# Performance work log

Hardware: AMD Instinct MI355X
Metric: run time of the kernel (lower is better)

Reference implementation:

```python
import jax, jax.numpy as jnp
import numpy as np

EPS = 1e-6
RES_CONN = True


def _layernorm(x, g, b):
    mu = jnp.mean(x, axis=-1, keepdims=True)
    var = jnp.var(x, axis=-1, keepdims=True)
    return (x - mu) * jax.lax.rsqrt(var + EPS) * g + b


def setup_inputs() -> dict:
    key = jax.random.key(0)
    ks = jax.random.split(key, 8)
    L, H, V, B, T = 2, 1024, 32000, 4, 512
    s = 0.02
    return {
        "x": jax.random.randint(ks[0], (B, T), 0, V, dtype=jnp.int32),
        "emb": jax.random.normal(ks[1], (V, H), jnp.float32) * s,
        "ln_g": jnp.ones((L, H), jnp.float32),
        "ln_b": jnp.zeros((L, H), jnp.float32),
        "Wl": jax.random.normal(ks[2], (L, 2 * H, 4 * H), jnp.float32) * s,
        "bl": jnp.zeros((L, 4 * H), jnp.float32),
        "Wo": jax.random.normal(ks[3], (L, H, H), jnp.float32) * s,
        "bo": jnp.zeros((L, H), jnp.float32),
        "W1": jax.random.normal(ks[4], (L, H, 4 * H), jnp.float32) * s,
        "b1": jnp.zeros((L, 4 * H), jnp.float32),
        "W2": jax.random.normal(ks[5], (L, 4 * H, H), jnp.float32) * s,
        "b2": jnp.zeros((L, H), jnp.float32),
    }


def reference(x, emb, ln_g, ln_b, Wl, bl, Wo, bo, W1, b1, W2, b2):
    # x: [B, T] int token ids. Returns dec_logits [B, T, V].
    B, T = x.shape
    L, H = ln_g.shape
    x_emb = emb[x]                      # [B, T, H] (dropout inactive: eval mode)
    xs = jnp.swapaxes(x_emb, 0, 1)      # [T, B, H]

    def step(carry, xt):
        c_prev, h_prev = carry          # each [L, B, H]
        cs, hs = [], []
        prev_input = jnp.zeros_like(xt)
        inp = xt                        # [B, H]
        for m in range(L):
            xn = _layernorm(inp, ln_g[m], ln_b[m])
            z = jnp.concatenate([xn, h_prev[m]], axis=-1) @ Wl[m] + bl[m]
            z = z.reshape(B, 4, H)
            i_g = jax.nn.sigmoid(z[:, 0])
            f_g = jax.nn.sigmoid(z[:, 1])
            o_g = jax.nn.sigmoid(z[:, 2])
            c = f_g * c_prev[m] + i_g * jnp.tanh(z[:, 3])
            h = o_g * jnp.tanh(c)
            ff = jax.nn.relu(xn @ W1[m] + b1[m]) @ W2[m] + b2[m]
            y = inp + ff + h @ Wo[m] + bo[m]
            if RES_CONN:
                y = y + prev_input
            prev_input = inp
            inp = y
            cs.append(c)
            hs.append(h)
        logits = inp @ emb.T            # tied embedding: [B, V]
        return (jnp.stack(cs), jnp.stack(hs)), logits

    carry0 = (jnp.zeros((L, B, H), x_emb.dtype), jnp.zeros((L, B, H), x_emb.dtype))
    _, logits = jax.lax.scan(step, carry0, xs)   # logits [T, B, V]
    return jnp.swapaxes(logits, 0, 1)            # [B, T, V]
```

## Files before the change

### kernel.cpp

```cpp
#include <hip/hip_runtime.h>

typedef unsigned short u16;
typedef short bf16x8 __attribute__((ext_vector_type(8)));
typedef unsigned short ushort8 __attribute__((ext_vector_type(8)));
typedef unsigned short us4 __attribute__((ext_vector_type(4)));
typedef unsigned u32x4 __attribute__((ext_vector_type(4)));
typedef float fx4 __attribute__((ext_vector_type(4)));

#define DEVI __device__ __forceinline__

enum { BB = 4, TT = 512, HH = 1024, VV = 32000, H4 = 4096 };
enum { WSTR = 1032 };

DEVI u16 f2bf(float f) {
    union { float f; unsigned u; } x; x.f = f;
    unsigned r = x.u + 0x7fff + ((x.u >> 16) & 1);
    return (u16)(r >> 16);
}
DEVI float bf2f(u16 u) {
    union { unsigned u; float f; } x; x.u = ((unsigned)u) << 16;
    return x.f;
}
DEVI float sigm(float x) { return 1.f / (1.f + __expf(-x)); }
DEVI float tanh_f(float x) {
    float a = fabsf(x);
    float t = 1.f - 2.f / (__expf(2.f * a) + 1.f);
    return x < 0.f ? -t : t;
}

DEVI unsigned ald_u32(const unsigned* p) { return __hip_atomic_load(p, __ATOMIC_RELAXED, __HIP_MEMORY_SCOPE_AGENT); }
DEVI void ast_u32(unsigned* p, unsigned v) { __hip_atomic_store(p, v, __ATOMIC_RELAXED, __HIP_MEMORY_SCOPE_AGENT); }

DEVI void ld4cc(const unsigned* p, u32x4* out) {
    asm volatile("global_load_dwordx4 %0, %1, off sc0 sc1" : "=v"(*out) : "v"(p));
}

template <int SLP>
DEVI void sent_poll(const unsigned* sbase, unsigned want, int lane) {
    const unsigned* p = sbase + lane;
    unsigned v = ald_u32(p);
    while (v != want) { __builtin_amdgcn_s_sleep(SLP); v = ald_u32(p); }
}
DEVI void data_fetch(const unsigned* dbase, u16* st, int tid) {
    u32x4 d;
    ld4cc(dbase + tid * 4, &d);
    asm volatile("s_waitcnt vmcnt(0)" ::: "memory");
    __builtin_amdgcn_sched_barrier(0);
    int wi = tid * 8;
    u16* dst = st + (wi >> 10) * WSTR + (wi & 1023);
    *(us4*)dst       = (us4){(u16)d[0], (u16)(d[0] >> 16), (u16)d[1], (u16)(d[1] >> 16)};
    *(us4*)(dst + 4) = (us4){(u16)d[2], (u16)(d[2] >> 16), (u16)d[3], (u16)(d[3] >> 16)};
}

template <int SLP>
DEVI void poll4096(const unsigned* base, unsigned want, u16* st, int tid) {
    const unsigned* p0 = base + tid * 8;
    const unsigned* p1 = p0 + 4;
    u32x4 v0, v1;
    ld4cc(p0, &v0); ld4cc(p1, &v1);
    asm volatile("s_waitcnt vmcnt(0)" ::: "memory");
    __builtin_amdgcn_sched_barrier(0);
    for (;;) {
        bool o0 = ((v0[0]>>16)==want)&((v0[1]>>16)==want)&((v0[2]>>16)==want)&((v0[3]>>16)==want);
        bool o1 = ((v1[0]>>16)==want)&((v1[1]>>16)==want)&((v1[2]>>16)==want)&((v1[3]>>16)==want);
        if (o0 & o1) break;
        __builtin_amdgcn_s_sleep(SLP);
        if (!o0) ld4cc(p0, &v0);
        if (!o1) ld4cc(p1, &v1);
        asm volatile("s_waitcnt vmcnt(0)" ::: "memory");
        __builtin_amdgcn_sched_barrier(0);
    }
    int wi = tid * 8;
    u16* d = st + (wi >> 10) * WSTR + (wi & 1023);
    *(us4*)d       = (us4){(u16)v0[0], (u16)v0[1], (u16)v0[2], (u16)v0[3]};
    *(us4*)(d + 4) = (us4){(u16)v1[0], (u16)v1[1], (u16)v1[2], (u16)v1[3]};
}

DEVI unsigned poll_word(const unsigned* p, unsigned want) {
    unsigned v = ald_u32(p);
    while ((v >> 16) != want) { __builtin_amdgcn_s_sleep(2); v = ald_u32(p); }
    return v & 0xFFFFu;
}

DEVI void gates64(const u16* wl, const u16* st, float* fb, int tid) {
    int lane = tid & 63, wv = tid >> 6;
    int rt = wv & 3, kh = wv >> 2;
    fx4 acc = {0.f, 0.f, 0.f, 0.f};
    int aoff = (rt * 16 + (lane & 15)) * WSTR + (lane >> 4) * 8;
    int boff = (lane & 3) * WSTR + (lane >> 4) * 8;
#pragma unroll
    for (int kt = 0; kt < 16; kt++) {
        int k0 = (kh * 16 + kt) * 32;
        bf16x8 a = *(const bf16x8*)(wl + aoff + k0);
        bf16x8 b = *(const bf16x8*)(st + boff + k0);
        acc = __builtin_amdgcn_mfma_f32_16x16x32_bf16(a, b, acc, 0, 0, 0);
    }
    int col = lane & 15;
    if (col < 4) {
        int r0 = rt * 16 + (lane >> 4) * 4;
#pragma unroll
        for (int ri = 0; ri < 4; ri++) fb[kh * 256 + (r0 + ri) * 4 + col] = acc[ri];
    }
}

__global__ void transpose_cast(const float* __restrict__ src, u16* __restrict__ dst, int R, int C) {
    __shared__ float tile[32][33];
    int c0 = blockIdx.x * 32, r0 = blockIdx.y * 32;
    int x = threadIdx.x, y = threadIdx.y;
#pragma unroll
    for (int i = 0; i < 32; i += 8) tile[y + i][x] = src[(size_t)(r0 + y + i) * C + c0 + x];
    __syncthreads();
#pragma unroll
    for (int i = 0; i < 32; i += 8) dst[(size_t)(c0 + y + i) * R + r0 + x] = f2bf(tile[x][y + i]);
}

__global__ void cast_bf16(const float* __restrict__ src, u16* __restrict__ dst, int n) {
    int i = blockIdx.x * 256 + threadIdx.x;
    if (i < n) dst[i] = f2bf(src[i]);
}

__global__ void zero_buf(float* p, int n) {
    int i = blockIdx.x * 256 + threadIdx.x;
    if (i < n) p[i] = 0.f;
}

__global__ __launch_bounds__(256) void gather_ln(const int* __restrict__ x, const float* __restrict__ emb,
                                                 const float* __restrict__ g, const float* __restrict__ b,
                                                 float* __restrict__ xe, u16* __restrict__ xn0) {
    int t = blockIdx.x, bb = blockIdx.y;
    int row = x[bb * TT + t];
    const float* e = emb + (size_t)row * HH;
    float v[4]; float s = 0.f, s2 = 0.f;
#pragma unroll
    for (int p = 0; p < 4; p++) { v[p] = e[p * 256 + threadIdx.x]; s += v[p]; s2 += v[p] * v[p]; }
    __shared__ float ls[4], ls2[4];
    for (int off = 32; off; off >>= 1) { s += __shfl_xor(s, off); s2 += __shfl_xor(s2, off); }
    int w = threadIdx.x >> 6, lane = threadIdx.x & 63;
    if (lane == 0) { ls[w] = s; ls2[w] = s2; }
    __syncthreads();
    s = ls[0] + ls[1] + ls[2] + ls[3];
    s2 = ls2[0] + ls2[1] + ls2[2] + ls2[3];
    float mu = s * (1.f / HH);
    float var = s2 * (1.f / HH) - mu * mu;
    float rs = rsqrtf(var + 1e-6f);
    size_t base = ((size_t)t * BB + bb) * HH;
#pragma unroll
    for (int p = 0; p < 4; p++) {
        int j = p * 256 + threadIdx.x;
        xe[base + j] = v[p];
        xn0[base + j] = f2bf((v[p] - mu) * rs * g[j] + b[j]);
    }
}

template <int MODE>
__global__ __launch_bounds__(256) void gemm_bt(const u16* __restrict__ A, const u16* __restrict__ Bt,
                                               float* __restrict__ Cf, u16* __restrict__ Cb,
                                               const float* __restrict__ bias, int M, int N, int K) {
    __shared__ u16 ldsA[128 * 40];
    __shared__ u16 ldsB[128 * 40];
    const int tid = threadIdx.x;
    const int m0 = blockIdx.y * 128, n0 = blockIdx.x * 128;
    const int lane = tid & 63, wid = tid >> 6;
    const int wr = wid >> 1, wc = wid & 1;
    const int l15 = lane & 15, lk = (lane >> 4) * 8;
    fx4 acc[4][4];
#pragma unroll
    for (int a = 0; a < 4; a++)
#pragma unroll
        for (int b = 0; b < 4; b++) { fx4 z = {0.f, 0.f, 0.f, 0.f}; acc[a][b] = z; }

    const int arow = tid >> 2, acol = (tid & 3) * 8;
    for (int k0 = 0; k0 < K; k0 += 32) {
#pragma unroll
        for (int p = 0; p < 2; p++) {
            int r = arow + p * 64;
            ushort8 va = *(const ushort8*)(A + (size_t)(m0 + r) * K + k0 + acol);
            *(ushort8*)&ldsA[r * 40 + acol] = va;
            ushort8 vb = *(const ushort8*)(Bt + (size_t)(n0 + r) * K + k0 + acol);
            *(ushort8*)&ldsB[r * 40 + acol] = vb;
        }
        __syncthreads();
        bf16x8 af[4], bfr[4];
#pragma unroll
        for (int mi = 0; mi < 4; mi++) af[mi] = *(const bf16x8*)&ldsA[(wr * 64 + mi * 16 + l15) * 40 + lk];
#pragma unroll
        for (int ni = 0; ni < 4; ni++) bfr[ni] = *(const bf16x8*)&ldsB[(wc * 64 + ni * 16 + l15) * 40 + lk];
#pragma unroll
        for (int mi = 0; mi < 4; mi++)
#pragma unroll
            for (int ni = 0; ni < 4; ni++)
                acc[mi][ni] = __builtin_amdgcn_mfma_f32_16x16x32_bf16(af[mi], bfr[ni], acc[mi][ni], 0, 0, 0);
        __syncthreads();
    }
#pragma unroll
    for (int mi = 0; mi < 4; mi++) {
#pragma unroll
        for (int ni = 0; ni < 4; ni++) {
#pragma unroll
            for (int r = 0; r < 4; r++) {
                int gr = m0 + wr * 64 + mi * 16 + (lane >> 4) * 4 + r;
                int gc = n0 + wc * 64 + ni * 16 + l15;
                float v = acc[mi][ni][r];
                if (MODE == 0) {
                    Cf[(size_t)gr * N + gc] = v + bias[gc];
                } else if (MODE == 1) {
                    float u = v + bias[gc];
                    Cb[(size_t)gr * N + gc] = f2bf(u > 0.f ? u : 0.f);
                } else if (MODE == 2) {
                    Cf[(size_t)gr * N + gc] += v;
                } else {
                    int b = gr & 3, t = gr >> 2;
                    Cf[((size_t)b * TT + t) * VV + gc] = v;
                }
            }
        }
    }
}

__global__ __launch_bounds__(512, 1) void lstm_pipe(
    const u16* __restrict__ Wh0T, const u16* __restrict__ Wo0T,
    const u16* __restrict__ Wx1T, const u16* __restrict__ Wh1T,
    const float* __restrict__ pz_all, const float* __restrict__ xe, const float* __restrict__ ff0,
    const float* __restrict__ lng, const float* __restrict__ lnb,
    const float* __restrict__ bl, const float* __restrict__ bo,
    float* __restrict__ y0_all, u16* __restrict__ xn1, u16* __restrict__ H1bf,
    unsigned* __restrict__ R) {
    __shared__ u16 wlds[64 * WSTR];
    __shared__ u16 stg[4 * WSTR];
    __shared__ float fb[1664];

    const int bid = blockIdx.x;
    const int tid = threadIdx.x;
    const int lane = tid & 63, wv = tid >> 6;

    unsigned* RD0 = R;
    unsigned* RS0 = R + 32768;
    unsigned* RD1 = R + 33792;
    unsigned* RS1 = R + 41984;
    unsigned* RPART = R + 42240;
    unsigned* RXN = R + 46336;
    unsigned* RZX = R + 111872;
    unsigned* PROGY = R + 374016;
    unsigned* PROGZX = R + 376064;
    unsigned* PROGL1 = R + 378112;

    if (bid < 64) {
        const int w = bid;
        {
            int row = tid >> 3, kc = tid & 7;
            int gr = (row >> 4) * 1024 + w * 16 + (row & 15);
            const uint4* s = (const uint4*)(Wh0T + (size_t)gr * 1024 + kc * 128);
            uint4* d = (uint4*)(wlds + row * WSTR + kc * 128);
#pragma unroll
            for (int i = 0; i < 16; i++) d[i] = s[i];
        }
        if (tid < 64) fb[1024 + tid] = 0.f;
        __syncthreads();

        for (int s = 0; s < TT; s++) {
            if ((s & 7) == 0 && tid < 64) {
                for (;;) {
                    unsigned p = ald_u32(PROGY + tid * 32);
#pragma unroll
                    for (int off = 1; off < 64; off <<= 1) {
                        unsigned o = (unsigned)__shfl_xor((int)p, off);
                        p = p < o ? p : o;
                    }
                    if ((int)p >= s - 8) break;
                    __builtin_amdgcn_s_sleep(8);
                }
            }
            float pzv[4] = {0.f, 0.f, 0.f, 0.f};
            if (tid < 64) {
                int x = tid >> 2, b = tid & 3;
#pragma unroll
                for (int g = 0; g < 4; g++)
                    pzv[g] = pz_all[((size_t)s * 4 + b) * 4096 + g * 1024 + w * 16 + x];
            }
            if (wv == 0) sent_poll<1>(RS0 + ((s + 15) & 15) * 64, (unsigned)s, lane);
            __syncthreads();
            data_fetch(RD0 + ((s + 15) & 15) * 2048, stg, tid);
            __syncthreads();
            float* gbuf = fb + (s & 1) * 512;
            gates64(wlds, stg, gbuf, tid);
            __syncthreads();
            if (tid < 64) {
                int x = tid >> 2, b = tid & 3;
                float z0 = gbuf[(0*16+x)*4+b] + gbuf[256+(0*16+x)*4+b] + pzv[0];
                float z1 = gbuf[(1*16+x)*4+b] + gbuf[256+(1*16+x)*4+b] + pzv[1];
                float z2 = gbuf[(2*16+x)*4+b] + gbuf[256+(2*16+x)*4+b] + pzv[2];
                float z3 = gbuf[(3*16+x)*4+b] + gbuf[256+(3*16+x)*4+b] + pzv[3];
                float ig = sigm(z0), fg = sigm(z1), og = sigm(z2), gg = tanh_f(z3);
                float c = fg * fb[1024 + tid] + ig * gg;
                fb[1024 + tid] = c;
                float h = og * tanh_f(c);
                float hn = __shfl(h, (tid + 4) & 63);
                if (((tid >> 2) & 1) == 0) {
                    int x = tid >> 2, b = tid & 3;
                    unsigned word = (unsigned)f2bf(h) | ((unsigned)f2bf(hn) << 16);
                    ast_u32(&RD0[(s & 15) * 2048 + b * 512 + w * 8 + (x >> 1)], word);
                }
                asm volatile("s_waitcnt vmcnt(0)" ::: "memory");
                if (tid == 0) ast_u32(&RS0[(s & 15) * 64 + w], (unsigned)(s + 1));
            }
        }
    } else if (bid < 128) {
        const int wy = bid - 64;
        {
            int row = tid >> 5, kc = tid & 31;
            const uint4* s = (const uint4*)(Wo0T + (size_t)(wy * 16 + row) * 1024 + kc * 32);
            uint4* d = (uint4*)(wlds + row * WSTR + kc * 32);
            d[0] = s[0]; d[1] = s[1]; d[2] = s[2]; d[3] = s[3];
        }
        float lgR = 0.f, lbR = 0.f, boR = 0.f;
        if (tid < 64) {
            int x = tid >> 2;
            lgR = lng[1024 + wy * 16 + x];
            lbR = lnb[1024 + wy * 16 + x];
            boR = bo[wy * 16 + x];
        }
        __syncthreads();

        for (int t = 0; t <= TT; t++) {
            const bool doDot = (t < TT);
            const bool doLN = (t >= 1);
            if ((t & 7) == 0 && tid < 64) {
                for (;;) {
                    unsigned p = ald_u32(PROGZX + tid * 32);
#pragma unroll
                    for (int off = 1; off < 64; off <<= 1) {
                        unsigned o = (unsigned)__shfl_xor((int)p, off);
                        p = p < o ? p : o;
                    }
                    if ((int)p >= t - 8) break;
                    __builtin_amdgcn_s_sleep(8);
                }
            }
            float xev = 0.f, ffv = 0.f;
            if (doDot && tid < 64) {
                int x = tid >> 2, b = tid & 3;
                size_t base = ((size_t)t * 4 + b) * 1024 + wy * 16 + x;
                xev = xe[base]; ffv = ff0[base];
            }
            if (doDot && wv == 0) sent_poll<4>(RS0 + (t & 15) * 64, (unsigned)(t + 1), lane);
            __syncthreads();
            if (doDot) data_fetch(RD0 + (t & 15) * 2048, stg, tid);
            if (doLN) {
                const unsigned* p = RPART + ((t - 1) & 3) * 1024 + tid * 2;
                unsigned hi = poll_word(p, (unsigned)t);
                unsigned lo = poll_word(p + 1, (unsigned)t);
                union { unsigned u; float f; } cv; cv.u = (hi << 16) | lo;
                fb[tid] = cv.f;
            }
            __syncthreads();
            if (doDot && tid == 0) ast_u32(PROGY + wy * 32, (unsigned)(t + 1));
            if (doLN && tid < 8) {
                int b = tid & 3, kind = tid >> 2;
                float S = 0.f;
                for (int i = 0; i < 64; i++) S += fb[i * 8 + b * 2 + kind];
                fb[704 + kind * 4 + b] = S;
            }
            if (doDot) {
                int out = tid >> 3, c = tid & 7;
                const u16* wrow = wlds + (out >> 2) * WSTR + c * 128;
                const u16* hrow = stg + (out & 3) * WSTR + c * 128;
                float acc = 0.f;
#pragma unroll
                for (int m = 0; m < 16; m++) {
                    ushort8 w8 = *(const ushort8*)(wrow + m * 8);
                    ushort8 h8 = *(const ushort8*)(hrow + m * 8);
#pragma unroll
                    for (int q = 0; q < 8; q++) acc += bf2f(w8[q]) * bf2f(h8[q]);
                }
                acc += __shfl_xor(acc, 1); acc += __shfl_xor(acc, 2); acc += __shfl_xor(acc, 4);
                if (c == 0) fb[512 + out] = acc;
            }
            __syncthreads();
            if (doDot && tid < 64) {
                int x = tid >> 2, b = tid & 3;
                float y = fb[512 + tid] + xev + ffv + boR;
                y0_all[((size_t)t * 4 + b) * 1024 + wy * 16 + x] = y;
                fb[576 + (t & 1) * 64 + tid] = y;
                float sv = y, sq = y * y;
#pragma unroll
                for (int off = 4; off < 64; off <<= 1) { sv += __shfl_xor(sv, off); sq += __shfl_xor(sq, off); }
                if (tid < 4) {
                    unsigned tg = (unsigned)(t + 1) << 16;
                    unsigned* pb = RPART + (t & 3) * 1024 + wy * 16 + tid * 4;
                    union { float f; unsigned u; } c1, c2; c1.f = sv; c2.f = sq;
                    ast_u32(pb + 0, tg | (c1.u >> 16));
                    ast_u32(pb + 1, tg | (c1.u & 0xFFFFu));
                    ast_u32(pb + 2, tg | (c2.u >> 16));
                    ast_u32(pb + 3, tg | (c2.u & 0xFFFFu));
                }
            }
            __syncthreads();
            if (doLN && tid < 64) {
                int x = tid >> 2, b = tid & 3;
                int u = t - 1;
                float mu = fb[704 + b] * (1.f / 1024.f);
                float rs = rsqrtf(fb[708 + b] * (1.f / 1024.f) - mu * mu + 1e-6f);
                float yv = fb[576 + (u & 1) * 64 + tid];
                float xnv = (yv - mu) * rs * lgR + lbR;
                u16 xb = f2bf(xnv);
                xn1[(size_t)u * 4096 + b * 1024 + wy * 16 + x] = xb;
                ast_u32(&RXN[(u & 15) * 4096 + b * 1024 + wy * 16 + x],
                        ((unsigned)(u + 1) << 16) | xb);
            }
        }
    } else if (bid < 192) {
        const int wz = bid - 128;
        {
            int row = tid >> 3, kc = tid & 7;
            int gr = (row >> 4) * 1024 + wz * 16 + (row & 15);
            const uint4* s = (const uint4*)(Wx1T + (size_t)gr * 1024 + kc * 128);
            uint4* d = (uint4*)(wlds + row * WSTR + kc * 128);
#pragma unroll
            for (int i = 0; i < 16; i++) d[i] = s[i];
        }
        if (tid < 64) fb[1536 + tid] = bl[4096 + (tid >> 4) * 1024 + wz * 16 + (tid & 15)];
        __syncthreads();

        for (int t = 0; t < TT; t++) {
            if ((t & 7) == 0 && tid == 0) {
                while ((int)ald_u32(PROGL1) < t - 6) __builtin_amdgcn_s_sleep(8);
            }
            poll4096<8>(RXN + (t & 15) * 4096, (unsigned)(t + 1), stg, tid);
            __syncthreads();
            gates64(wlds, stg, fb, tid);
            __syncthreads();
            if (tid == 0) ast_u32(PROGZX + wz * 32, (unsigned)(t + 1));
            if (tid < 256) {
                int lr = tid >> 2, b = tid & 3;
                float v = fb[lr * 4 + b] + fb[256 + lr * 4 + b] + fb[1536 + lr];
                ast_u32(&RZX[(t & 15) * 16384 + wz * 256 + tid],
                        ((unsigned)(t + 1) << 16) | f2bf(v));
            }
            __syncthreads();
        }
    } else {
        const int w1 = bid - 192;
        {
            int row = tid >> 3, kc = tid & 7;
            int gr = (row >> 4) * 1024 + w1 * 16 + (row & 15);
            const uint4* s = (const uint4*)(Wh1T + (size_t)gr * 1024 + kc * 128);
            uint4* d = (uint4*)(wlds + row * WSTR + kc * 128);
#pragma unroll
            for (int i = 0; i < 16; i++) d[i] = s[i];
        }
        if (tid < 64) fb[1600 + tid] = 0.f;
        __syncthreads();

        for (int v = 0; v < TT; v++) {
            if (tid < 256) {
                const unsigned* p = RZX + (v & 15) * 16384 + w1 * 256 + tid;
                fb[1024 + (v & 1) * 256 + tid] = bf2f((u16)poll_word(p, (unsigned)(v + 1)));
            }
            if (wv == 0) sent_poll<1>(RS1 + ((v + 3) & 3) * 64, (unsigned)v, lane);
            __syncthreads();
            data_fetch(RD1 + ((v + 3) & 3) * 2048, stg, tid);
            __syncthreads();
            if (bid == 192 && tid == 0) ast_u32(PROGL1, (unsigned)(v + 1));
            float* gbuf = fb + (v & 1) * 512;
            gates64(wlds, stg, gbuf, tid);
            __syncthreads();
            if (tid < 64) {
                int x = tid >> 2, b = tid & 3;
                const float* zb = fb + 1024 + (v & 1) * 256;
                float z0 = gbuf[(0*16+x)*4+b] + gbuf[256+(0*16+x)*4+b] + zb[(0*16+x)*4+b];
                float z1 = gbuf[(1*16+x)*4+b] + gbuf[256+(1*16+x)*4+b] + zb[(1*16+x)*4+b];
                float z2 = gbuf[(2*16+x)*4+b] + gbuf[256+(2*16+x)*4+b] + zb[(2*16+x)*4+b];
                float z3 = gbuf[(3*16+x)*4+b] + gbuf[256+(3*16+x)*4+b] + zb[(3*16+x)*4+b];
                float ig = sigm(z0), fg = sigm(z1), og = sigm(z2), gg = tanh_f(z3);
                float c = fg * fb[1600 + tid] + ig * gg;
                fb[1600 + tid] = c;
                float h = og * tanh_f(c);
                u16 hb = f2bf(h);
                H1bf[(size_t)v * 4096 + b * 1024 + w1 * 16 + x] = hb;
                float hn = __shfl(h, (tid + 4) & 63);
                if (((tid >> 2) & 1) == 0) {
                    unsigned word = (unsigned)hb | ((unsigned)f2bf(hn) << 16);
                    ast_u32(&RD1[(v & 3) * 2048 + b * 512 + w1 * 8 + ((tid >> 2) >> 1)], word);
                }
                asm volatile("s_waitcnt vmcnt(0)" ::: "memory");
                if (tid == 0) ast_u32(&RS1[(v & 3) * 64 + w1], (unsigned)(v + 1));
            }
        }
    }
}

__global__ void p1_add(float* __restrict__ y, const float* __restrict__ xe,
                       const float* __restrict__ b2_1, const float* __restrict__ bo_1) {
    int idx = blockIdx.x * 256 + threadIdx.x;
    int j = idx & (HH - 1);
    y[idx] += xe[idx] + b2_1[j] + bo_1[j];
}

__global__ void p2_cast(const float* __restrict__ y, u16* __restrict__ o) {
    int idx = blockIdx.x * 256 + threadIdx.x;
    o[idx] = f2bf(y[idx]);
}

extern "C" void kernel_launch(void* const* d_in, const int* in_sizes, int n_in,
                              void* d_out, int out_size, void* d_ws, size_t ws_size,
                              hipStream_t stream) {
    const int* x = (const int*)d_in[0];
    const float* emb = (const float*)d_in[1];
    const float* ln_g = (const float*)d_in[2];
    const float* ln_b = (const float*)d_in[3];
    const float* Wl = (const float*)d_in[4];
    const float* bl = (const float*)d_in[5];
    const float* Wo = (const float*)d_in[6];
    const float* bo = (const float*)d_in[7];
    const float* W1 = (const float*)d_in[8];
    const float* b1 = (const float*)d_in[9];
    const float* W2 = (const float*)d_in[10];
    const float* b2 = (const float*)d_in[11];
    float* out = (float*)d_out;

    char* wp = (char*)d_ws;
    auto alloc = [&](size_t bytes) { void* p = wp; wp += (bytes + 255) & ~(size_t)255; return p; };
    const size_t MBT = (size_t)TT * BB;
    float* xe     = (float*)alloc(MBT * HH * 4);
    float* pre_z0 = (float*)alloc(MBT * H4 * 4);
    float* ff0    = (float*)alloc(MBT * HH * 4);
    float* y0_all = (float*)alloc(MBT * HH * 4);
    u16* xn0      = (u16*)alloc(MBT * HH * 2);
    u16* xn1      = (u16*)alloc(MBT * HH * 2);
    u16* U0       = (u16*)alloc(MBT * H4 * 2);
    u16* U1       = (u16*)alloc(MBT * H4 * 2);
    u16* H1bf     = (u16*)alloc(MBT * HH * 2);
    u16* Y1bf     = (u16*)alloc(MBT * HH * 2);
    unsigned* R   = (unsigned*)alloc(378144 * 4);
    u16* WlxT0 = (u16*)alloc((size_t)H4 * HH * 2);
    u16* WlhT0 = (u16*)alloc((size_t)H4 * HH * 2);
    u16* WlxT1 = (u16*)alloc((size_t)H4 * HH * 2);
    u16* WlhT1 = (u16*)alloc((size_t)H4 * HH * 2);
    u16* Wo0T  = (u16*)alloc((size_t)HH * HH * 2);
    u16* Wo1T  = (u16*)alloc((size_t)HH * HH * 2);
    u16* W10T  = (u16*)alloc((size_t)H4 * HH * 2);
    u16* W11T  = (u16*)alloc((size_t)H4 * HH * 2);
    u16* W20T  = (u16*)alloc((size_t)HH * H4 * 2);
    u16* W21T  = (u16*)alloc((size_t)HH * H4 * 2);
    u16* embB  = (u16*)alloc((size_t)VV * HH * 2);

    dim3 tb(32, 8);
    transpose_cast<<<dim3(128, 32), tb, 0, stream>>>(Wl, WlxT0, HH, H4);
    transpose_cast<<<dim3(128, 32), tb, 0, stream>>>(Wl + 1024 * 4096, WlhT0, HH, H4);
    transpose_cast<<<dim3(128, 32), tb, 0, stream>>>(Wl + 2048 * 4096, WlxT1, HH, H4);
    transpose_cast<<<dim3(128, 32), tb, 0, stream>>>(Wl + 3072 * 4096, WlhT1, HH, H4);
    transpose_cast<<<dim3(32, 32), tb, 0, stream>>>(Wo, Wo0T, HH, HH);
    transpose_cast<<<dim3(32, 32), tb, 0, stream>>>(Wo + 1024 * 1024, Wo1T, HH, HH);
    transpose_cast<<<dim3(128, 32), tb, 0, stream>>>(W1, W10T, HH, H4);
    transpose_cast<<<dim3(128, 32), tb, 0, stream>>>(W1 + 1024 * 4096, W11T, HH, H4);
    transpose_cast<<<dim3(32, 128), tb, 0, stream>>>(W2, W20T, H4, HH);
    transpose_cast<<<dim3(32, 128), tb, 0, stream>>>(W2 + 4096 * 1024, W21T, H4, HH);
    cast_bf16<<<(VV * HH + 255) / 256, 256, 0, stream>>>(emb, embB, VV * HH);
    gather_ln<<<dim3(TT, BB), 256, 0, stream>>>(x, emb, ln_g, ln_b, xe, xn0);

    gemm_bt<0><<<dim3(32, 16), 256, 0, stream>>>(xn0, WlxT0, pre_z0, nullptr, bl, 2048, 4096, 1024);
    gemm_bt<1><<<dim3(32, 16), 256, 0, stream>>>(xn0, W10T, nullptr, U0, b1, 2048, 4096, 1024);
    gemm_bt<0><<<dim3(8, 16), 256, 0, stream>>>(U0, W20T, ff0, nullptr, b2, 2048, 1024, 4096);

    zero_buf<<<1478, 256, 0, stream>>>((float*)R, 378144);

    lstm_pipe<<<256, 512, 0, stream>>>(WlhT0, Wo0T, WlxT1, WlhT1, pre_z0, xe, ff0,
                                       ln_g, ln_b, bl, bo, y0_all, xn1, H1bf, R);

    gemm_bt<1><<<dim3(32, 16), 256, 0, stream>>>(xn1, W11T, nullptr, U1, b1 + 4096, 2048, 4096, 1024);
    p1_add<<<8192, 256, 0, stream>>>(y0_all, xe, b2 + 1024, bo + 1024);
    gemm_bt<2><<<dim3(8, 16), 256, 0, stream>>>(U1, W21T, y0_all, nullptr, nullptr, 2048, 1024, 4096);
    gemm_bt<2><<<dim3(8, 16), 256, 0, stream>>>(H1bf, Wo1T, y0_all, nullptr, nullptr, 2048, 1024, 1024);
    p2_cast<<<8192, 256, 0, stream>>>(y0_all, Y1bf);
    gemm_bt<3><<<dim3(250, 16), 256, 0, stream>>>(Y1bf, embB, out, nullptr, nullptr, 2048, 32000, 1024);
}
```

Measured before the change: 3.641 ms.

## Use direct global-to-LDS loads in GEMM and fuse epilogue add/cast kernels

The GEMM tile loads now go straight from global memory into LDS via global_load_lds, dropping the register round-trip, and the padded LDS stride is removed. Two elementwise kernels are removed: the residual/bias add moves into the W2 GEMM epilogue, and the bf16 cast of y moves into the Wo GEMM epilogue. The LSTM progress polling now uses wave 1 instead of wave 0, presumably so it overlaps with the wave 0 sentinel poll. Without the LDS padding, the MFMA fragment reads may hit more bank conflicts.

```diff
diff --git a/kernel.cpp b/kernel.cpp
--- a/kernel.cpp
+++ b/kernel.cpp
@@ -33,6 +33,11 @@
 
 DEVI void ld4cc(const unsigned* p, u32x4* out) {
     asm volatile("global_load_dwordx4 %0, %1, off sc0 sc1" : "=v"(*out) : "v"(p));
+}
+
+DEVI void gl_lds16(const u16* g, u16* l) {
+    __builtin_amdgcn_global_load_lds((const __attribute__((address_space(1))) unsigned*)g,
+                                     (__attribute__((address_space(3))) unsigned*)l, 16, 0, 0);
 }
 
 template <int SLP>
@@ -155,9 +160,10 @@
 template <int MODE>
 __global__ __launch_bounds__(256) void gemm_bt(const u16* __restrict__ A, const u16* __restrict__ Bt,
                                                float* __restrict__ Cf, u16* __restrict__ Cb,
-                                               const float* __restrict__ bias, int M, int N, int K) {
-    __shared__ u16 ldsA[128 * 40];
-    __shared__ u16 ldsB[128 * 40];
+                                               const float* __restrict__ bias, const float* __restrict__ bias2,
+                                               const float* __restrict__ addf, int M, int N, int K) {
+    __shared__ u16 ldsA[128 * 32];
+    __shared__ u16 ldsB[128 * 32];
     const int tid = threadIdx.x;
     const int m0 = blockIdx.y * 128, n0 = blockIdx.x * 128;
     const int lane = tid & 63, wid = tid >> 6;
@@ -169,22 +175,19 @@
 #pragma unroll
         for (int b = 0; b < 4; b++) { fx4 z = {0.f, 0.f, 0.f, 0.f}; acc[a][b] = z; }
 
-    const int arow = tid >> 2, acol = (tid & 3) * 8;
+    const int srow = lane >> 2, scol = (lane & 3) * 8;
+    const int i0 = wid * 32;
     for (int k0 = 0; k0 < K; k0 += 32) {
-#pragma unroll
-        for (int p = 0; p < 2; p++) {
-            int r = arow + p * 64;
-            ushort8 va = *(const ushort8*)(A + (size_t)(m0 + r) * K + k0 + acol);
-            *(ushort8*)&ldsA[r * 40 + acol] = va;
-            ushort8 vb = *(const ushort8*)(Bt + (size_t)(n0 + r) * K + k0 + acol);
-            *(ushort8*)&ldsB[r * 40 + acol] = vb;
-        }
+        gl_lds16(A + (size_t)(m0 + i0 + srow) * K + k0 + scol,       &ldsA[i0 * 32]);
+        gl_lds16(A + (size_t)(m0 + i0 + 16 + srow) * K + k0 + scol,  &ldsA[(i0 + 16) * 32]);
+        gl_lds16(Bt + (size_t)(n0 + i0 + srow) * K + k0 + scol,      &ldsB[i0 * 32]);
+        gl_lds16(Bt + (size_t)(n0 + i0 + 16 + srow) * K + k0 + scol, &ldsB[(i0 + 16) * 32]);
         __syncthreads();
         bf16x8 af[4], bfr[4];
 #pragma unroll
-        for (int mi = 0; mi < 4; mi++) af[mi] = *(const bf16x8*)&ldsA[(wr * 64 + mi * 16 + l15) * 40 + lk];
-#pragma unroll
-        for (int ni = 0; ni < 4; ni++) bfr[ni] = *(const bf16x8*)&ldsB[(wc * 64 + ni * 16 + l15) * 40 + lk];
+        for (int mi = 0; mi < 4; mi++) af[mi] = *(const bf16x8*)&ldsA[(wr * 64 + mi * 16 + l15) * 32 + lk];
+#pragma unroll
+        for (int ni = 0; ni < 4; ni++) bfr[ni] = *(const bf16x8*)&ldsB[(wc * 64 + ni * 16 + l15) * 32 + lk];
 #pragma unroll
         for (int mi = 0; mi < 4; mi++)
 #pragma unroll
@@ -201,16 +204,19 @@
                 int gr = m0 + wr * 64 + mi * 16 + (lane >> 4) * 4 + r;
                 int gc = n0 + wc * 64 + ni * 16 + l15;
                 float v = acc[mi][ni][r];
+                size_t idx = (size_t)gr * N + gc;
                 if (MODE == 0) {
-                    Cf[(size_t)gr * N + gc] = v + bias[gc];
+                    Cf[idx] = v + bias[gc];
                 } else if (MODE == 1) {
                     float u = v + bias[gc];
-                    Cb[(size_t)gr * N + gc] = f2bf(u > 0.f ? u : 0.f);
-                } else if (MODE == 2) {
-                    Cf[(size_t)gr * N + gc] += v;
-                } else {
+                    Cb[idx] = f2bf(u > 0.f ? u : 0.f);
+                } else if (MODE == 3) {
                     int b = gr & 3, t = gr >> 2;
                     Cf[((size_t)b * TT + t) * VV + gc] = v;
+                } else if (MODE == 4) {
+                    Cf[idx] += v + addf[idx] + bias[gc] + bias2[gc];
+                } else {
+                    Cb[idx] = f2bf(Cf[idx] + v);
                 }
             }
         }
@@ -258,9 +264,9 @@
         __syncthreads();
 
         for (int s = 0; s < TT; s++) {
-            if ((s & 7) == 0 && tid < 64) {
+            if ((s & 7) == 0 && wv == 1) {
                 for (;;) {
-                    unsigned p = ald_u32(PROGY + tid * 32);
+                    unsigned p = ald_u32(PROGY + lane * 32);
 #pragma unroll
                     for (int off = 1; off < 64; off <<= 1) {
                         unsigned o = (unsigned)__shfl_xor((int)p, off);
@@ -296,7 +302,6 @@
                 float h = og * tanh_f(c);
                 float hn = __shfl(h, (tid + 4) & 63);
                 if (((tid >> 2) & 1) == 0) {
-                    int x = tid >> 2, b = tid & 3;
                     unsigned word = (unsigned)f2bf(h) | ((unsigned)f2bf(hn) << 16);
                     ast_u32(&RD0[(s & 15) * 2048 + b * 512 + w * 8 + (x >> 1)], word);
                 }
@@ -324,9 +329,9 @@
         for (int t = 0; t <= TT; t++) {
             const bool doDot = (t < TT);
             const bool doLN = (t >= 1);
-            if ((t & 7) == 0 && tid < 64) {
+            if ((t & 7) == 0 && wv == 1) {
                 for (;;) {
-                    unsigned p = ald_u32(PROGZX + tid * 32);
+                    unsigned p = ald_u32(PROGZX + lane * 32);
 #pragma unroll
                     for (int off = 1; off < 64; off <<= 1) {
                         unsigned o = (unsigned)__shfl_xor((int)p, off);
@@ -487,18 +492,6 @@
             }
         }
     }
-}
-
-__global__ void p1_add(float* __restrict__ y, const float* __restrict__ xe,
-                       const float* __restrict__ b2_1, const float* __restrict__ bo_1) {
-    int idx = blockIdx.x * 256 + threadIdx.x;
-    int j = idx & (HH - 1);
-    y[idx] += xe[idx] + b2_1[j] + bo_1[j];
-}
-
-__global__ void p2_cast(const float* __restrict__ y, u16* __restrict__ o) {
-    int idx = blockIdx.x * 256 + threadIdx.x;
-    o[idx] = f2bf(y[idx]);
 }
 
 extern "C" void kernel_launch(void* const* d_in, const int* in_sizes, int n_in,
@@ -558,19 +551,17 @@
     cast_bf16<<<(VV * HH + 255) / 256, 256, 0, stream>>>(emb, embB, VV * HH);
     gather_ln<<<dim3(TT, BB), 256, 0, stream>>>(x, emb, ln_g, ln_b, xe, xn0);
 
-    gemm_bt<0><<<dim3(32, 16), 256, 0, stream>>>(xn0, WlxT0, pre_z0, nullptr, bl, 2048, 4096, 1024);
-    gemm_bt<1><<<dim3(32, 16), 256, 0, stream>>>(xn0, W10T, nullptr, U0, b1, 2048, 4096, 1024);
-    gemm_bt<0><<<dim3(8, 16), 256, 0, stream>>>(U0, W20T, ff0, nullptr, b2, 2048, 1024, 4096);
+    gemm_bt<0><<<dim3(32, 16), 256, 0, stream>>>(xn0, WlxT0, pre_z0, nullptr, bl, nullptr, nullptr, 2048, 4096, 1024);
+    gemm_bt<1><<<dim3(32, 16), 256, 0, stream>>>(xn0, W10T, nullptr, U0, b1, nullptr, nullptr, 2048, 4096, 1024);
+    gemm_bt<0><<<dim3(8, 16), 256, 0, stream>>>(U0, W20T, ff0, nullptr, b2, nullptr, nullptr, 2048, 1024, 4096);
 
     zero_buf<<<1478, 256, 0, stream>>>((float*)R, 378144);
 
     lstm_pipe<<<256, 512, 0, stream>>>(WlhT0, Wo0T, WlxT1, WlhT1, pre_z0, xe, ff0,
                                        ln_g, ln_b, bl, bo, y0_all, xn1, H1bf, R);
 
-    gemm_bt<1><<<dim3(32, 16), 256, 0, stream>>>(xn1, W11T, nullptr, U1, b1 + 4096, 2048, 4096, 1024);
-    p1_add<<<8192, 256, 0, stream>>>(y0_all, xe, b2 + 1024, bo + 1024);
-    gemm_bt<2><<<dim3(8, 16), 256, 0, stream>>>(U1, W21T, y0_all, nullptr, nullptr, 2048, 1024, 4096);
-    gemm_bt<2><<<dim3(8, 16), 256, 0, stream>>>(H1bf, Wo1T, y0_all, nullptr, nullptr, 2048, 1024, 1024);
-    p2_cast<<<8192, 256, 0, stream>>>(y0_all, Y1bf);
-    gemm_bt<3><<<dim3(250, 16), 256, 0, stream>>>(Y1bf, embB, out, nullptr, nullptr, 2048, 32000, 1024);
-}
+    gemm_bt<1><<<dim3(32, 16), 256, 0, stream>>>(xn1, W11T, nullptr, U1, b1 + 4096, nullptr, nullptr, 2048, 4096, 1024);
+    gemm_bt<4><<<dim3(8, 16), 256, 0, stream>>>(U1, W21T, y0_all, nullptr, b2 + 1024, bo + 1024, xe, 2048, 1024, 4096);
+    gemm_bt<5><<<dim3(8, 16), 256, 0, stream>>>(H1bf, Wo1T, y0_all, Y1bf, nullptr, nullptr, nullptr, 2048, 1024, 1024);
+    gemm_bt<3><<<dim3(250, 16), 256, 0, stream>>>(Y1bf, embB, out, nullptr, nullptr, nullptr, nullptr, 2048, 32000, 1024);
+}
```

Result: faster. 3.560 ms (-2.2%).
